# Performance work log

Measured on AMD Instinct MI355X. Metric: run time of the kernel, lower is better.

The kernel has to match this reference:

```python
import jax, jax.numpy as jnp
import numpy as np

N_NODES = 100000
N_EDGES = 1600000
IN_CH, HID_CH, OUT_CH = 512, 256, 64
K = 10
ALPHA = 0.1


def setup_inputs() -> dict:
    key = jax.random.key(0)
    k1, k2, k3, k4 = jax.random.split(key, 4)
    x = jax.random.normal(k1, (N_NODES, IN_CH), dtype=jnp.float32)
    edge_index = jax.random.randint(k2, (2, N_EDGES), 0, N_NODES, dtype=jnp.int64)
    w1 = jax.random.normal(k3, (IN_CH, HID_CH), dtype=jnp.float32) * 0.02
    b1 = jnp.zeros((HID_CH,), dtype=jnp.float32)
    w2 = jax.random.normal(k4, (HID_CH, OUT_CH), dtype=jnp.float32) * 0.02
    b2 = jnp.zeros((OUT_CH,), dtype=jnp.float32)
    return {"x": x, "edge_index": edge_index, "w1": w1, "b1": b1, "w2": w2, "b2": b2}


def reference(x, edge_index, w1, b1, w2, b2):
    n = x.shape[0]
    # MLP (dropout is identity in eval mode)
    h = jax.nn.relu(x @ w1 + b1)
    h = h @ w2 + b2  # [N, out]

    # GCN normalization with added self-loops (PyG gcn_norm)
    loops = jnp.arange(n, dtype=edge_index.dtype)
    src = jnp.concatenate([edge_index[0], loops])  # message sources (row)
    dst = jnp.concatenate([edge_index[1], loops])  # message targets (col)
    ones = jnp.ones(src.shape[0], dtype=h.dtype)
    deg = jax.ops.segment_sum(ones, dst, num_segments=n)
    dinv = jnp.where(deg > 0, jax.lax.rsqrt(deg), 0.0)
    norm = dinv[src] * dinv[dst]  # [E+N]

    h0 = h

    def step(hc, _):
        msg = jax.ops.segment_sum(norm[:, None] * hc[src], dst, num_segments=n)
        return (1.0 - ALPHA) * msg + ALPHA * h0, None

    h, _ = jax.lax.scan(step, h, None, length=K)
    return h
```

## Files before the change

### kernel.cpp

```cpp
#include <hip/hip_runtime.h>
#include <hip/hip_bf16.h>


typedef __attribute__((ext_vector_type(8))) short short8;
typedef __attribute__((ext_vector_type(4))) float floatx4;
typedef __attribute__((ext_vector_type(8))) _Float16 half8;

#define IN_CH 512
#define HID_CH 256
#define OUT_CH 64

static __device__ __forceinline__ unsigned short bf16_bits(float f) {
    __hip_bfloat16 b = __float2bfloat16(f);
    union { __hip_bfloat16 b; unsigned short u; } u2; u2.b = b; return u2.u;
}

typedef __attribute__((address_space(3))) unsigned int lds_u32;
typedef __attribute__((address_space(1))) const unsigned int glb_u32;

static __device__ __forceinline__ void gload16(const void* g, void* l) {
    __builtin_amdgcn_global_load_lds((glb_u32*)g, (lds_u32*)l, 16, 0, 0);
}

__global__ void k_probe(const int* __restrict__ e, long long ewords,
                        const unsigned short* __restrict__ xw,
                        int* __restrict__ meta) {
    if (blockIdx.x == 16) {
        int any = 0;
        long long half = ewords >> 1;
        long long step = half / 4096; if (step < 1) step = 1;
        for (long long i = threadIdx.x; i < 4096; i += blockDim.x) {
            long long idx = 2 * (i * step) + 1;
            if (idx < ewords) any |= e[idx];
        }
        if (any) atomicOr(&meta[0], 1);
    } else {
        const short8* x8 = (const short8*)xw;
        int bad = 0;
        for (int i = blockIdx.x * 256 + threadIdx.x; i < 8192; i += 4096) {
            short8 v = x8[i];
#pragma unroll
            for (int j = 0; j < 8; ++j) {
                unsigned short w = (unsigned short)v[j];
                if ((w & 0x7F80) == 0x7F80) bad = 1;
            }
        }
        if (bad) atomicOr(&meta[1], 1);
    }
}

__global__ void k_transpose(const void* __restrict__ w,
                            __hip_bfloat16* __restrict__ wt, int K, int N,
                            const int* __restrict__ meta) {
    int f32 = meta[1];
    int i = blockIdx.x * blockDim.x + threadIdx.x;
    if (i < K * N) {
        int k = i / N, n = i - k * N;
        __hip_bfloat16 v = f32 ? __float2bfloat16(((const float*)w)[i])
                               : ((const __hip_bfloat16*)w)[i];
        wt[n * K + k] = v;
    }
}

__global__ void k_count(const int* __restrict__ e, const int* __restrict__ meta,
                        int E, int* __restrict__ cnt, int* __restrict__ rank, int n) {
    int is32 = meta[0];
    int j = blockIdx.x * 256 + threadIdx.x;
    if (j < E) {
        long long idx = (long long)E + j;
        int d = is32 ? e[idx] : (int)((const long long*)e)[idx];
        if ((unsigned)d >= (unsigned)n) d = 0;
        rank[j] = atomicAdd(&cnt[d], 1);
    }
}

__global__ __launch_bounds__(1024) void k_scan1(const int* __restrict__ cnt,
                                                int* __restrict__ incl,
                                                int* __restrict__ bsum, int n) {
    __shared__ int s[1024];
    int i = blockIdx.x * 1024 + threadIdx.x;
    int v = (i < n) ? cnt[i] : 0;
    s[threadIdx.x] = v;
    __syncthreads();
    for (int off = 1; off < 1024; off <<= 1) {
        int t = (threadIdx.x >= off) ? s[threadIdx.x - off] : 0;
        __syncthreads();
        s[threadIdx.x] += t;
        __syncthreads();
    }
    incl[blockIdx.x * 1024 + threadIdx.x] = s[threadIdx.x];
    if (threadIdx.x == 1023) bsum[blockIdx.x] = s[1023];
}

__global__ void k_scan2(const int* __restrict__ bsum, int* __restrict__ boff, int nb) {
    if (blockIdx.x == 0 && threadIdx.x == 0) {
        int a = 0;
        for (int i = 0; i < nb; ++i) { boff[i] = a; a += bsum[i]; }
    }
}

__global__ void k_scan3(const int* __restrict__ incl, const int* __restrict__ cnt,
                        const int* __restrict__ boff, int* __restrict__ rowptr,
                        int n, int E) {
    int i = blockIdx.x * 256 + threadIdx.x;
    if (i < n) rowptr[i] = incl[i] - cnt[i] + boff[i >> 10];
    if (i == 0) rowptr[n] = E;
}

__global__ void k_dinv(const int* __restrict__ cnt, float* __restrict__ dinv, int n) {
    int i = blockIdx.x * 256 + threadIdx.x;
    if (i < n) dinv[i] = rsqrtf((float)cnt[i] + 1.0f);
}

__global__ void k_fill(const int* __restrict__ e, const int* __restrict__ meta, int E,
                       const int* __restrict__ rowptr, const int* __restrict__ rank,
                       int* __restrict__ col, int n) {
    int is32 = meta[0];
    int j = blockIdx.x * 256 + threadIdx.x;
    if (j < E) {
        int s, d;
        if (is32) { s = e[j]; d = e[(long long)E + j]; }
        else {
            const long long* e64 = (const long long*)e;
            s = (int)e64[j]; d = (int)e64[(long long)E + j];
        }
        if ((unsigned)s >= (unsigned)n) s = 0;
        if ((unsigned)d >= (unsigned)n) d = 0;
        col[rowptr[d] + rank[j]] = s;
    }
}

__global__ __launch_bounds__(256, 4) void k_gemm1(
    const void* __restrict__ A, const __hip_bfloat16* __restrict__ Bt,
    const void* __restrict__ bias, __hip_bfloat16* __restrict__ C,
    int M, const int* __restrict__ meta)
{
    __shared__ __attribute__((aligned(16))) char lds[24576];
    const int f32 = meta[1];
    const int t = threadIdx.x;
    const int bm = blockIdx.x * 64, bn = blockIdx.y * 128;
    const int wave = t >> 6, lane = t & 63;
    const int wm = (wave & 1) * 32, wn = (wave >> 1) * 64;
    const int quad = lane >> 4, l16 = lane & 15;
    const int lrow = lane >> 3;
    const int lcol = ((lane & 7) ^ lrow) * 8;

    floatx4 acc[2][4];
#pragma unroll
    for (int i = 0; i < 2; ++i)
#pragma unroll
        for (int j = 0; j < 4; ++j) acc[i][j] = {0.f, 0.f, 0.f, 0.f};

    const __hip_bfloat16* Ab = (const __hip_bfloat16*)A;
    const float* Af = (const float*)A;

    for (int k0 = 0; k0 < IN_CH; k0 += 64) {
        __syncthreads();
#pragma unroll
        for (int i = 0; i < 4; ++i) {
            int s = wave * 4 + i;
            gload16(Bt + (size_t)(bn + 8 * s + lrow) * IN_CH + k0 + lcol,
                    lds + 8192 + s * 1024);
        }
        if (f32) {
#pragma unroll
            for (int i = 0; i < 2; ++i) {
                int s = wave * 2 + i;
                int gr = bm + 8 * s + lrow; if (gr >= M) gr = M - 1;
                const float* src = Af + (size_t)gr * IN_CH + k0 + lcol;
                float4 a = *(const float4*)src;
                float4 b = *(const float4*)(src + 4);
                union { short8 s8; unsigned short us[8]; } u;
                u.us[0] = bf16_bits(a.x); u.us[1] = bf16_bits(a.y);
                u.us[2] = bf16_bits(a.z); u.us[3] = bf16_bits(a.w);
                u.us[4] = bf16_bits(b.x); u.us[5] = bf16_bits(b.y);
                u.us[6] = bf16_bits(b.z); u.us[7] = bf16_bits(b.w);
                *(short8*)(lds + s * 1024 + lane * 16) = u.s8;
            }
        } else {
#pragma unroll
            for (int i = 0; i < 2; ++i) {
                int s = wave * 2 + i;
                int gr = bm + 8 * s + lrow; if (gr >= M) gr = M - 1;
                gload16(Ab + (size_t)gr * IN_CH + k0 + lcol, lds + s * 1024);
            }
        }
        __syncthreads();
#pragma unroll
        for (int kk = 0; kk < 64; kk += 32) {
            const int cb = kk * 2 + quad * 16;
            short8 af[2], bf[4];
#pragma unroll
            for (int i = 0; i < 2; ++i) {
                int r = wm + i * 16 + l16;
                af[i] = *(const short8*)(lds + r * 128 + (cb ^ ((r & 7) << 4)));
            }
#pragma unroll
            for (int j = 0; j < 4; ++j) {
                int r = wn + j * 16 + l16;
                bf[j] = *(const short8*)(lds + 8192 + r * 128 + (cb ^ ((r & 7) << 4)));
            }
#pragma unroll
            for (int i = 0; i < 2; ++i)
#pragma unroll
                for (int j = 0; j < 4; ++j)
                    acc[i][j] = __builtin_amdgcn_mfma_f32_16x16x32_bf16(af[i], bf[j], acc[i][j], 0, 0, 0);
        }
    }

#pragma unroll
    for (int i = 0; i < 2; ++i)
#pragma unroll
        for (int j = 0; j < 4; ++j) {
            int nn = bn + wn + j * 16 + l16;
            float bv = f32 ? ((const float*)bias)[nn]
                           : __bfloat162float(((const __hip_bfloat16*)bias)[nn]);
#pragma unroll
            for (int r = 0; r < 4; ++r) {
                int m = bm + wm + i * 16 + quad * 4 + r;
                if (m < M)
                    C[(size_t)m * HID_CH + nn] = __float2bfloat16(fmaxf(acc[i][j][r] + bv, 0.f));
            }
        }
}

__global__ __launch_bounds__(256) void k_gemm2(
    const __hip_bfloat16* __restrict__ A, const __hip_bfloat16* __restrict__ Bt,
    const void* __restrict__ bias, const float* __restrict__ dinv,
    _Float16* __restrict__ h0h, _Float16* __restrict__ g0,
    int M, const int* __restrict__ meta)
{
    __shared__ __attribute__((aligned(16))) short As[64 * 72];
    __shared__ __attribute__((aligned(16))) short Bs[64 * 72];
    const int f32 = meta[1];
    const int t = threadIdx.x;
    const int bm = blockIdx.x * 64;
    const int wave = t >> 6, lane = t & 63;
    const int wm = (wave >> 1) * 32, wn = (wave & 1) * 32;
    const int quad = lane >> 4, l16 = lane & 15;

    floatx4 acc[2][2];
#pragma unroll
    for (int i = 0; i < 2; ++i)
#pragma unroll
        for (int j = 0; j < 2; ++j) acc[i][j] = {0.f, 0.f, 0.f, 0.f};

    for (int k0 = 0; k0 < HID_CH; k0 += 64) {
        __syncthreads();
        for (int ch = t; ch < 1024; ch += 256) {
            int row = (ch & 511) >> 3, off = (ch & 7) * 8;
            if (ch < 512) {
                uint4 av = {0u, 0u, 0u, 0u};
                int gr = bm + row;
                if (gr < M)
                    av = *(const uint4*)((const char*)A + ((size_t)gr * HID_CH + k0 + off) * 2);
                *(uint4*)((char*)As + row * 144 + off * 2) = av;
            } else {
                uint4 bv = *(const uint4*)((const char*)Bt + ((size_t)row * HID_CH + k0 + off) * 2);
                *(uint4*)((char*)Bs + row * 144 + off * 2) = bv;
            }
        }
        __syncthreads();
#pragma unroll
        for (int kk = 0; kk < 64; kk += 32) {
            short8 af[2], bf[2];
#pragma unroll
            for (int i = 0; i < 2; ++i)
                af[i] = *(const short8*)((const char*)As + (wm + i * 16 + l16) * 144 + (kk + quad * 8) * 2);
#pragma unroll
            for (int j = 0; j < 2; ++j)
                bf[j] = *(const short8*)((const char*)Bs + (wn + j * 16 + l16) * 144 + (kk + quad * 8) * 2);
#pragma unroll
            for (int i = 0; i < 2; ++i)
#pragma unroll
                for (int j = 0; j < 2; ++j)
                    acc[i][j] = __builtin_amdgcn_mfma_f32_16x16x32_bf16(af[i], bf[j], acc[i][j], 0, 0, 0);
        }
    }

#pragma unroll
    for (int i = 0; i < 2; ++i) {
#pragma unroll
        for (int j = 0; j < 2; ++j) {
            int nn = wn + j * 16 + l16;
            float bv = f32 ? ((const float*)bias)[nn]
                           : __bfloat162float(((const __hip_bfloat16*)bias)[nn]);
#pragma unroll
            for (int r = 0; r < 4; ++r) {
                int m = bm + wm + i * 16 + quad * 4 + r;
                if (m < M) {
                    float v = acc[i][j][r] + bv;
                    float dv = dinv[m];
                    h0h[(size_t)m * OUT_CH + nn] = (_Float16)v;
                    g0[(size_t)m * OUT_CH + nn] = (_Float16)(dv * v);
                }
            }
        }
    }
}

template<int FINAL>
__global__ __launch_bounds__(256) void k_prop(
    const _Float16* __restrict__ g, const _Float16* __restrict__ h0h,
    const int* __restrict__ rowptr, const int* __restrict__ col,
    const float* __restrict__ dinv,
    _Float16* __restrict__ gout, void* __restrict__ outfinal, int n,
    const int* __restrict__ meta)
{
    int gid = blockIdx.x * 32 + (threadIdx.x >> 3);
    if (gid >= n) return;
    int lane = threadIdx.x & 7;
    const half8* g8 = (const half8*)g;

    half8 sv = g8[(size_t)gid * 8 + lane];
    float acc[8];
#pragma unroll
    for (int i = 0; i < 8; ++i) acc[i] = (float)sv[i];

    int e0 = rowptr[gid], e1 = rowptr[gid + 1];
    int e = e0;
    for (; e + 8 <= e1; e += 8) {
        int c[8];
#pragma unroll
        for (int u = 0; u < 8; ++u) c[u] = col[e + u];
        half8 v[8];
#pragma unroll
        for (int u = 0; u < 8; ++u) v[u] = g8[(size_t)c[u] * 8 + lane];
#pragma unroll
        for (int u = 0; u < 8; ++u)
#pragma unroll
            for (int i = 0; i < 8; ++i) acc[i] += (float)v[u][i];
    }
    for (; e + 4 <= e1; e += 4) {
        int c0 = col[e], c1 = col[e + 1], c2 = col[e + 2], c3 = col[e + 3];
        half8 v0 = g8[(size_t)c0 * 8 + lane];
        half8 v1 = g8[(size_t)c1 * 8 + lane];
        half8 v2 = g8[(size_t)c2 * 8 + lane];
        half8 v3 = g8[(size_t)c3 * 8 + lane];
#pragma unroll
        for (int i = 0; i < 8; ++i)
            acc[i] += ((float)v0[i] + (float)v1[i]) + ((float)v2[i] + (float)v3[i]);
    }
    for (; e < e1; ++e) {
        half8 v = g8[(size_t)col[e] * 8 + lane];
#pragma unroll
        for (int i = 0; i < 8; ++i) acc[i] += (float)v[i];
    }

    float dv = dinv[gid];
    half8 z = ((const half8*)h0h)[(size_t)gid * 8 + lane];

    if (FINAL) {
        float o[8];
#pragma unroll
        for (int i = 0; i < 8; ++i) o[i] = 0.9f * dv * acc[i] + 0.1f * (float)z[i];
        if (meta[1]) {
            float* of = (float*)outfinal + (size_t)gid * OUT_CH + lane * 8;
            float4 a = {o[0], o[1], o[2], o[3]}, b = {o[4], o[5], o[6], o[7]};
            *(float4*)of = a; *(float4*)(of + 4) = b;
        } else {
            struct alignas(16) BF8 { unsigned short v[8]; } ob;
#pragma unroll
            for (int i = 0; i < 8; ++i) ob.v[i] = bf16_bits(o[i]);
            *(BF8*)((unsigned short*)outfinal + (size_t)gid * OUT_CH + lane * 8) = ob;
        }
    } else {
        float w2v = 0.9f * dv * dv, w1v = 0.1f * dv;
        half8 o;
#pragma unroll
        for (int i = 0; i < 8; ++i) o[i] = (_Float16)(w2v * acc[i] + w1v * (float)z[i]);
        ((half8*)gout)[(size_t)gid * 8 + lane] = o;
    }
}

extern "C" void kernel_launch(void* const* d_in, const int* in_sizes, int n_in,
                              void* d_out, int out_size, void* d_ws, size_t ws_size,
                              hipStream_t stream) {
    const void* x    = d_in[0];
    const int* edges = (const int*)d_in[1];
    const void* w1   = d_in[2];
    const void* b1   = d_in[3];
    const void* w2   = d_in[4];
    const void* b2   = d_in[5];

    const int N = in_sizes[0] / IN_CH;
    const int E = in_sizes[1] / 2;
    const int NB = (N + 1023) / 1024;

    size_t off = 0;
    auto carve = [&](size_t bytes) -> void* {
        void* r = (char*)d_ws + off;
        off += (bytes + 255) & ~(size_t)255;
        return r;
    };
    __hip_bfloat16* h1  = (__hip_bfloat16*)carve((size_t)N * HID_CH * 2);
    _Float16* h0h       = (_Float16*)carve((size_t)N * OUT_CH * 2);
    _Float16* gA        = (_Float16*)carve((size_t)N * OUT_CH * 2);
    _Float16* gB        = (_Float16*)carve((size_t)N * OUT_CH * 2);
    __hip_bfloat16* w1t = (__hip_bfloat16*)carve((size_t)IN_CH * HID_CH * 2);
    __hip_bfloat16* w2t = (__hip_bfloat16*)carve((size_t)HID_CH * OUT_CH * 2);
    int* cnt            = (int*)carve((size_t)N * 4);
    int* incl           = (int*)carve((size_t)NB * 1024 * 4);
    int* bsum           = (int*)carve(1024 * 4);
    int* boff           = (int*)carve(1024 * 4);
    int* rowptr         = (int*)carve((size_t)(N + 1) * 4);
    float* dinv         = (float*)carve((size_t)N * 4);
    int* col            = (int*)carve((size_t)E * 4);
    int* meta           = (int*)carve(256);
    if (off > ws_size) return;

    int* rank = (int*)h1;

    hipMemsetAsync(cnt, 0, (size_t)N * 4, stream);
    hipMemsetAsync(meta, 0, 8, stream);

    k_probe<<<17, 256, 0, stream>>>(edges, (long long)2 * E,
                                    (const unsigned short*)x, meta);

    k_transpose<<<(IN_CH * HID_CH + 255) / 256, 256, 0, stream>>>(w1, w1t, IN_CH, HID_CH, meta);
    k_transpose<<<(HID_CH * OUT_CH + 255) / 256, 256, 0, stream>>>(w2, w2t, HID_CH, OUT_CH, meta);

    const int EB = (E + 255) / 256;
    k_count<<<EB, 256, 0, stream>>>(edges, meta, E, cnt, rank, N);
    k_scan1<<<NB, 1024, 0, stream>>>(cnt, incl, bsum, N);
    k_scan2<<<1, 64, 0, stream>>>(bsum, boff, NB);
    k_scan3<<<(N + 255) / 256, 256, 0, stream>>>(incl, cnt, boff, rowptr, N, E);
    k_dinv<<<(N + 255) / 256, 256, 0, stream>>>(cnt, dinv, N);
    k_fill<<<EB, 256, 0, stream>>>(edges, meta, E, rowptr, rank, col, N);

    dim3 g1((N + 63) / 64, 2);
    k_gemm1<<<g1, 256, 0, stream>>>(x, w1t, b1, h1, N, meta);
    const int MB = (N + 63) / 64;
    k_gemm2<<<MB, 256, 0, stream>>>(h1, w2t, b2, dinv, h0h, gA, N, meta);

    const int PB = (N + 31) / 32;
    const _Float16* cur = gA;
    _Float16* nxt = gB;
    for (int it = 0; it < 10; ++it) {
        if (it < 9) {
            k_prop<0><<<PB, 256, 0, stream>>>(cur, h0h, rowptr, col, dinv, nxt, nullptr, N, meta);
            const _Float16* tmp = cur; cur = nxt; nxt = (_Float16*)tmp;
        } else {
            k_prop<1><<<PB, 256, 0, stream>>>(cur, h0h, rowptr, col, dinv, nullptr, d_out, N, meta);
        }
    }
}
```

Baseline: 828.1 us.

## Double-buffer LDS tiles in first GEMM to overlap global loads with MFMA

Restructures the first MLP GEMM's K loop into a two-stage software pipeline. LDS grows to hold two A and two B tiles, and the next tile's global loads are issued before computing on the current one. Explicit vmcnt/lgkmcnt waits and raw s_barriers replace __syncthreads. The aim is to hide global memory latency behind MFMA work, at the cost of doubled LDS per block, which may reduce occupancy, and fragile hand-counted waitcnt values.

```diff
diff --git a/kernel.cpp b/kernel.cpp
--- a/kernel.cpp
+++ b/kernel.cpp
@@ -135,7 +135,7 @@
     const void* __restrict__ bias, __hip_bfloat16* __restrict__ C,
     int M, const int* __restrict__ meta)
 {
-    __shared__ __attribute__((aligned(16))) char lds[24576];
+    __shared__ __attribute__((aligned(16))) char lds[49152];
     const int f32 = meta[1];
     const int t = threadIdx.x;
     const int bm = blockIdx.x * 64, bn = blockIdx.y * 128;
@@ -153,60 +153,141 @@
 
     const __hip_bfloat16* Ab = (const __hip_bfloat16*)A;
     const float* Af = (const float*)A;
-
-    for (int k0 = 0; k0 < IN_CH; k0 += 64) {
-        __syncthreads();
-#pragma unroll
-        for (int i = 0; i < 4; ++i) {
-            int s = wave * 4 + i;
-            gload16(Bt + (size_t)(bn + 8 * s + lrow) * IN_CH + k0 + lcol,
-                    lds + 8192 + s * 1024);
-        }
-        if (f32) {
-#pragma unroll
-            for (int i = 0; i < 2; ++i) {
-                int s = wave * 2 + i;
-                int gr = bm + 8 * s + lrow; if (gr >= M) gr = M - 1;
-                const float* src = Af + (size_t)gr * IN_CH + k0 + lcol;
-                float4 a = *(const float4*)src;
-                float4 b = *(const float4*)(src + 4);
+    const int NT = IN_CH / 64;
+
+    const int s0 = wave * 2, s1 = wave * 2 + 1;
+    int gr0 = bm + 8 * s0 + lrow; if (gr0 >= M) gr0 = M - 1;
+    int gr1 = bm + 8 * s1 + lrow; if (gr1 >= M) gr1 = M - 1;
+
+#define ABUF(p) (lds + (p) * 8192)
+#define BBUF(p) (lds + 16384 + (p) * 16384)
+
+    if (f32) {
+        float4 ar0a, ar0b, ar1a, ar1b;
+        {
+            const float* src0 = Af + (size_t)gr0 * IN_CH + lcol;
+            const float* src1 = Af + (size_t)gr1 * IN_CH + lcol;
+            float4 a0 = *(const float4*)src0, b0 = *(const float4*)(src0 + 4);
+            float4 a1 = *(const float4*)src1, b1 = *(const float4*)(src1 + 4);
+#pragma unroll
+            for (int i = 0; i < 4; ++i)
+                gload16(Bt + (size_t)(bn + 8 * (wave * 4 + i) + lrow) * IN_CH + lcol,
+                        BBUF(0) + (wave * 4 + i) * 1024);
+            union { short8 s8; unsigned short us[8]; } u;
+            u.us[0] = bf16_bits(a0.x); u.us[1] = bf16_bits(a0.y);
+            u.us[2] = bf16_bits(a0.z); u.us[3] = bf16_bits(a0.w);
+            u.us[4] = bf16_bits(b0.x); u.us[5] = bf16_bits(b0.y);
+            u.us[6] = bf16_bits(b0.z); u.us[7] = bf16_bits(b0.w);
+            *(short8*)(ABUF(0) + s0 * 1024 + lane * 16) = u.s8;
+            u.us[0] = bf16_bits(a1.x); u.us[1] = bf16_bits(a1.y);
+            u.us[2] = bf16_bits(a1.z); u.us[3] = bf16_bits(a1.w);
+            u.us[4] = bf16_bits(b1.x); u.us[5] = bf16_bits(b1.y);
+            u.us[6] = bf16_bits(b1.z); u.us[7] = bf16_bits(b1.w);
+            *(short8*)(ABUF(0) + s1 * 1024 + lane * 16) = u.s8;
+        }
+        for (int kt = 0; kt < NT; ++kt) {
+            const int p = kt & 1;
+            const int k0n = (kt + 1) * 64;
+            if (kt + 1 < NT) {
+                const float* src0 = Af + (size_t)gr0 * IN_CH + k0n + lcol;
+                const float* src1 = Af + (size_t)gr1 * IN_CH + k0n + lcol;
+                ar0a = *(const float4*)src0; ar0b = *(const float4*)(src0 + 4);
+                ar1a = *(const float4*)src1; ar1b = *(const float4*)(src1 + 4);
+#pragma unroll
+                for (int i = 0; i < 4; ++i)
+                    gload16(Bt + (size_t)(bn + 8 * (wave * 4 + i) + lrow) * IN_CH + k0n + lcol,
+                            BBUF(p ^ 1) + (wave * 4 + i) * 1024);
+                asm volatile("s_waitcnt vmcnt(8)" ::: "memory");
+            } else {
+                asm volatile("s_waitcnt vmcnt(0)" ::: "memory");
+            }
+            asm volatile("s_waitcnt lgkmcnt(0)" ::: "memory");
+            __builtin_amdgcn_sched_barrier(0);
+            __builtin_amdgcn_s_barrier();
+#pragma unroll
+            for (int kk = 0; kk < 64; kk += 32) {
+                const int cb = kk * 2 + quad * 16;
+                short8 af[2], bf[4];
+#pragma unroll
+                for (int i = 0; i < 2; ++i) {
+                    int r = wm + i * 16 + l16;
+                    af[i] = *(const short8*)(ABUF(p) + r * 128 + (cb ^ ((r & 7) << 4)));
+                }
+#pragma unroll
+                for (int j = 0; j < 4; ++j) {
+                    int r = wn + j * 16 + l16;
+                    bf[j] = *(const short8*)(BBUF(p) + r * 128 + (cb ^ ((r & 7) << 4)));
+                }
+#pragma unroll
+                for (int i = 0; i < 2; ++i)
+#pragma unroll
+                    for (int j = 0; j < 4; ++j)
+                        acc[i][j] = __builtin_amdgcn_mfma_f32_16x16x32_bf16(af[i], bf[j], acc[i][j], 0, 0, 0);
+            }
+            if (kt + 1 < NT) {
                 union { short8 s8; unsigned short us[8]; } u;
-                u.us[0] = bf16_bits(a.x); u.us[1] = bf16_bits(a.y);
-                u.us[2] = bf16_bits(a.z); u.us[3] = bf16_bits(a.w);
-                u.us[4] = bf16_bits(b.x); u.us[5] = bf16_bits(b.y);
-                u.us[6] = bf16_bits(b.z); u.us[7] = bf16_bits(b.w);
-                *(short8*)(lds + s * 1024 + lane * 16) = u.s8;
-            }
-        } else {
-#pragma unroll
-            for (int i = 0; i < 2; ++i) {
-                int s = wave * 2 + i;
-                int gr = bm + 8 * s + lrow; if (gr >= M) gr = M - 1;
-                gload16(Ab + (size_t)gr * IN_CH + k0 + lcol, lds + s * 1024);
-            }
-        }
-        __syncthreads();
-#pragma unroll
-        for (int kk = 0; kk < 64; kk += 32) {
-            const int cb = kk * 2 + quad * 16;
-            short8 af[2], bf[4];
-#pragma unroll
-            for (int i = 0; i < 2; ++i) {
-                int r = wm + i * 16 + l16;
-                af[i] = *(const short8*)(lds + r * 128 + (cb ^ ((r & 7) << 4)));
-            }
-#pragma unroll
-            for (int j = 0; j < 4; ++j) {
-                int r = wn + j * 16 + l16;
-                bf[j] = *(const short8*)(lds + 8192 + r * 128 + (cb ^ ((r & 7) << 4)));
-            }
-#pragma unroll
-            for (int i = 0; i < 2; ++i)
-#pragma unroll
-                for (int j = 0; j < 4; ++j)
-                    acc[i][j] = __builtin_amdgcn_mfma_f32_16x16x32_bf16(af[i], bf[j], acc[i][j], 0, 0, 0);
-        }
-    }
+                u.us[0] = bf16_bits(ar0a.x); u.us[1] = bf16_bits(ar0a.y);
+                u.us[2] = bf16_bits(ar0a.z); u.us[3] = bf16_bits(ar0a.w);
+                u.us[4] = bf16_bits(ar0b.x); u.us[5] = bf16_bits(ar0b.y);
+                u.us[6] = bf16_bits(ar0b.z); u.us[7] = bf16_bits(ar0b.w);
+                *(short8*)(ABUF(p ^ 1) + s0 * 1024 + lane * 16) = u.s8;
+                u.us[0] = bf16_bits(ar1a.x); u.us[1] = bf16_bits(ar1a.y);
+                u.us[2] = bf16_bits(ar1a.z); u.us[3] = bf16_bits(ar1a.w);
+                u.us[4] = bf16_bits(ar1b.x); u.us[5] = bf16_bits(ar1b.y);
+                u.us[6] = bf16_bits(ar1b.z); u.us[7] = bf16_bits(ar1b.w);
+                *(short8*)(ABUF(p ^ 1) + s1 * 1024 + lane * 16) = u.s8;
+            }
+            __builtin_amdgcn_s_barrier();
+        }
+    } else {
+#pragma unroll
+        for (int i = 0; i < 4; ++i)
+            gload16(Bt + (size_t)(bn + 8 * (wave * 4 + i) + lrow) * IN_CH + lcol,
+                    BBUF(0) + (wave * 4 + i) * 1024);
+        gload16(Ab + (size_t)gr0 * IN_CH + lcol, ABUF(0) + s0 * 1024);
+        gload16(Ab + (size_t)gr1 * IN_CH + lcol, ABUF(0) + s1 * 1024);
+        for (int kt = 0; kt < NT; ++kt) {
+            const int p = kt & 1;
+            const int k0n = (kt + 1) * 64;
+            if (kt + 1 < NT) {
+#pragma unroll
+                for (int i = 0; i < 4; ++i)
+                    gload16(Bt + (size_t)(bn + 8 * (wave * 4 + i) + lrow) * IN_CH + k0n + lcol,
+                            BBUF(p ^ 1) + (wave * 4 + i) * 1024);
+                gload16(Ab + (size_t)gr0 * IN_CH + k0n + lcol, ABUF(p ^ 1) + s0 * 1024);
+                gload16(Ab + (size_t)gr1 * IN_CH + k0n + lcol, ABUF(p ^ 1) + s1 * 1024);
+                asm volatile("s_waitcnt vmcnt(6)" ::: "memory");
+            } else {
+                asm volatile("s_waitcnt vmcnt(0)" ::: "memory");
+            }
+            asm volatile("s_waitcnt lgkmcnt(0)" ::: "memory");
+            __builtin_amdgcn_sched_barrier(0);
+            __builtin_amdgcn_s_barrier();
+#pragma unroll
+            for (int kk = 0; kk < 64; kk += 32) {
+                const int cb = kk * 2 + quad * 16;
+                short8 af[2], bf[4];
+#pragma unroll
+                for (int i = 0; i < 2; ++i) {
+                    int r = wm + i * 16 + l16;
+                    af[i] = *(const short8*)(ABUF(p) + r * 128 + (cb ^ ((r & 7) << 4)));
+                }
+#pragma unroll
+                for (int j = 0; j < 4; ++j) {
+                    int r = wn + j * 16 + l16;
+                    bf[j] = *(const short8*)(BBUF(p) + r * 128 + (cb ^ ((r & 7) << 4)));
+                }
+#pragma unroll
+                for (int i = 0; i < 2; ++i)
+#pragma unroll
+                    for (int j = 0; j < 4; ++j)
+                        acc[i][j] = __builtin_amdgcn_mfma_f32_16x16x32_bf16(af[i], bf[j], acc[i][j], 0, 0, 0);
+            }
+            __builtin_amdgcn_s_barrier();
+        }
+    }
+#undef ABUF
+#undef BBUF
 
 #pragma unroll
     for (int i = 0; i < 2; ++i)
```

New measurement: 838.0 us. Within noise of the previous version (+1.2%).

## Make gemm1 tile cover full hidden width so x is read once

Applied to the files above, without the earlier changes.

The first GEMM now uses 128-row blocks of 1024 threads that compute all 256 hidden columns, instead of 64x128 tiles over a 2D grid. The input x matrix, which is large and stored in fp32, is then read from global memory once rather than twice. This should roughly halve gemm1's dominant HBM traffic. The trade-offs are a doubled LDS footprint of 48KB and a launch bound of (1024, 4), which may push register limits low enough to cause spills and may reduce occupancy.

```diff
diff --git a/kernel.cpp b/kernel.cpp
--- a/kernel.cpp
+++ b/kernel.cpp
@@ -130,17 +130,17 @@
     }
 }
 
-__global__ __launch_bounds__(256, 4) void k_gemm1(
+__global__ __launch_bounds__(1024, 4) void k_gemm1(
     const void* __restrict__ A, const __hip_bfloat16* __restrict__ Bt,
     const void* __restrict__ bias, __hip_bfloat16* __restrict__ C,
     int M, const int* __restrict__ meta)
 {
-    __shared__ __attribute__((aligned(16))) char lds[24576];
+    __shared__ __attribute__((aligned(16))) char lds[49152];
     const int f32 = meta[1];
     const int t = threadIdx.x;
-    const int bm = blockIdx.x * 64, bn = blockIdx.y * 128;
+    const int bm = blockIdx.x * 128;
     const int wave = t >> 6, lane = t & 63;
-    const int wm = (wave & 1) * 32, wn = (wave >> 1) * 64;
+    const int wm = (wave & 3) * 32, wn = (wave >> 2) * 64;
     const int quad = lane >> 4, l16 = lane & 15;
     const int lrow = lane >> 3;
     const int lcol = ((lane & 7) ^ lrow) * 8;
@@ -154,36 +154,31 @@
     const __hip_bfloat16* Ab = (const __hip_bfloat16*)A;
     const float* Af = (const float*)A;
 
+#define ABASE (lds)
+#define BBASE (lds + 16384)
+
+    int gr = bm + 8 * wave + lrow; if (gr >= M) gr = M - 1;
+
     for (int k0 = 0; k0 < IN_CH; k0 += 64) {
         __syncthreads();
 #pragma unroll
-        for (int i = 0; i < 4; ++i) {
-            int s = wave * 4 + i;
-            gload16(Bt + (size_t)(bn + 8 * s + lrow) * IN_CH + k0 + lcol,
-                    lds + 8192 + s * 1024);
+        for (int i = 0; i < 2; ++i) {
+            int s = wave * 2 + i;
+            gload16(Bt + (size_t)(8 * s + lrow) * IN_CH + k0 + lcol,
+                    BBASE + s * 1024);
         }
         if (f32) {
-#pragma unroll
-            for (int i = 0; i < 2; ++i) {
-                int s = wave * 2 + i;
-                int gr = bm + 8 * s + lrow; if (gr >= M) gr = M - 1;
-                const float* src = Af + (size_t)gr * IN_CH + k0 + lcol;
-                float4 a = *(const float4*)src;
-                float4 b = *(const float4*)(src + 4);
-                union { short8 s8; unsigned short us[8]; } u;
-                u.us[0] = bf16_bits(a.x); u.us[1] = bf16_bits(a.y);
-                u.us[2] = bf16_bits(a.z); u.us[3] = bf16_bits(a.w);
-                u.us[4] = bf16_bits(b.x); u.us[5] = bf16_bits(b.y);
-                u.us[6] = bf16_bits(b.z); u.us[7] = bf16_bits(b.w);
-                *(short8*)(lds + s * 1024 + lane * 16) = u.s8;
-            }
+            const float* src = Af + (size_t)gr * IN_CH + k0 + lcol;
+            float4 a = *(const float4*)src;
+            float4 b = *(const float4*)(src + 4);
+            union { short8 s8; unsigned short us[8]; } u;
+            u.us[0] = bf16_bits(a.x); u.us[1] = bf16_bits(a.y);
+            u.us[2] = bf16_bits(a.z); u.us[3] = bf16_bits(a.w);
+            u.us[4] = bf16_bits(b.x); u.us[5] = bf16_bits(b.y);
+            u.us[6] = bf16_bits(b.z); u.us[7] = bf16_bits(b.w);
+            *(short8*)(ABASE + wave * 1024 + lane * 16) = u.s8;
         } else {
-#pragma unroll
-            for (int i = 0; i < 2; ++i) {
-                int s = wave * 2 + i;
-                int gr = bm + 8 * s + lrow; if (gr >= M) gr = M - 1;
-                gload16(Ab + (size_t)gr * IN_CH + k0 + lcol, lds + s * 1024);
-            }
+            gload16(Ab + (size_t)gr * IN_CH + k0 + lcol, ABASE + wave * 1024);
         }
         __syncthreads();
 #pragma unroll
@@ -193,12 +188,12 @@
 #pragma unroll
             for (int i = 0; i < 2; ++i) {
                 int r = wm + i * 16 + l16;
-                af[i] = *(const short8*)(lds + r * 128 + (cb ^ ((r & 7) << 4)));
+                af[i] = *(const short8*)(ABASE + r * 128 + (cb ^ ((r & 7) << 4)));
             }
 #pragma unroll
             for (int j = 0; j < 4; ++j) {
                 int r = wn + j * 16 + l16;
-                bf[j] = *(const short8*)(lds + 8192 + r * 128 + (cb ^ ((r & 7) << 4)));
+                bf[j] = *(const short8*)(BBASE + r * 128 + (cb ^ ((r & 7) << 4)));
             }
 #pragma unroll
             for (int i = 0; i < 2; ++i)
@@ -207,12 +202,14 @@
                     acc[i][j] = __builtin_amdgcn_mfma_f32_16x16x32_bf16(af[i], bf[j], acc[i][j], 0, 0, 0);
         }
     }
+#undef ABASE
+#undef BBASE
 
 #pragma unroll
     for (int i = 0; i < 2; ++i)
 #pragma unroll
         for (int j = 0; j < 4; ++j) {
-            int nn = bn + wn + j * 16 + l16;
+            int nn = wn + j * 16 + l16;
             float bv = f32 ? ((const float*)bias)[nn]
                            : __bfloat162float(((const __hip_bfloat16*)bias)[nn]);
 #pragma unroll
@@ -428,8 +425,8 @@
     k_dinv<<<(N + 255) / 256, 256, 0, stream>>>(cnt, dinv, N);
     k_fill<<<EB, 256, 0, stream>>>(edges, meta, E, rowptr, rank, col, N);
 
-    dim3 g1((N + 63) / 64, 2);
-    k_gemm1<<<g1, 256, 0, stream>>>(x, w1t, b1, h1, N, meta);
+    const int MB1 = (N + 127) / 128;
+    k_gemm1<<<MB1, 1024, 0, stream>>>(x, w1t, b1, h1, N, meta);
     const int MB = (N + 63) / 64;
     k_gemm2<<<MB, 256, 0, stream>>>(h1, w2t, b2, dinv, h0h, gA, N, meta);
 
```

Measured after the change: 815.1 us. Within noise of the previous version (-1.6%).
